# Performance work log

Hardware: AMD Instinct MI355X
Metric: run time of the kernel (lower is better)

The kernel has to match this reference:

```python
import jax, jax.numpy as jnp
import numpy as np

SEQLEN, BATCH, FEAT = 512, 64, 512
HID, WIN, LAYERS, OUT, NSPK = 1024, 16, 3, 512, 2


def setup_inputs() -> dict:
    key = jax.random.key(0)
    ks = jax.random.split(key, 16)
    s = 0.05  # small init scale to keep activations stable
    return {
        "h": jax.random.normal(ks[0], (SEQLEN, BATCH, FEAT), jnp.float32),
        "Wa": jax.random.normal(ks[1], (NSPK, HID, FEAT), jnp.float32) * s,
        "Wih0": jax.random.normal(ks[2], (4 * HID, FEAT), jnp.float32) * s,
        "Whh0": jax.random.normal(ks[3], (4 * HID, HID), jnp.float32) * s,
        "bih0": jax.random.normal(ks[4], (4 * HID,), jnp.float32) * s,
        "bhh0": jax.random.normal(ks[5], (4 * HID,), jnp.float32) * s,
        "Wih_rest": jax.random.normal(ks[6], (LAYERS - 1, 4 * HID, HID), jnp.float32) * s,
        "Whh_rest": jax.random.normal(ks[7], (LAYERS - 1, 4 * HID, HID), jnp.float32) * s,
        "bih_rest": jax.random.normal(ks[8], (LAYERS - 1, 4 * HID), jnp.float32) * s,
        "bhh_rest": jax.random.normal(ks[9], (LAYERS - 1, 4 * HID), jnp.float32) * s,
        "Wfc": jax.random.normal(ks[10], (OUT, HID + FEAT), jnp.float32) * s,
        "bfc": jax.random.normal(ks[11], (OUT,), jnp.float32) * s,
        "s0": jax.random.normal(ks[12], (BATCH, HID), jnp.float32),
        "h0": jax.random.normal(ks[13], (LAYERS, BATCH, HID), jnp.float32),
        "c0": jax.random.normal(ks[14], (LAYERS, BATCH, HID), jnp.float32),
    }


def _lstm_cell(x, h_prev, c_prev, Wih, Whh, bih, bhh):
    # torch.nn.LSTMCell math; only the new h is consumed downstream
    g = x @ Wih.T + bih + h_prev @ Whh.T + bhh  # [B, 4H]
    i, f, gg, o = jnp.split(g, 4, axis=1)
    c_new = jax.nn.sigmoid(f) * c_prev + jax.nn.sigmoid(i) * jnp.tanh(gg)
    return jax.nn.sigmoid(o) * jnp.tanh(c_new)


def reference(h, Wa, Wih0, Whh0, bih0, bhh0, Wih_rest, Whh_rest, bih_rest, bhh_rest, Wfc, bfc, s0, h0, c0):
    T, B, F = h.shape
    win_len = 2 * WIN + 1
    pad = jnp.zeros((WIN, B, F), h.dtype)
    h_pad = jnp.concatenate([pad, h, pad], axis=0)  # [T+2W, B, F]

    def make_step(Wa_s):
        def step(s_prev, i):
            window = jax.lax.dynamic_slice(h_pad, (i, 0, 0), (win_len, B, F))  # [w,B,F]
            proj = s_prev @ Wa_s                       # [B,F]
            e = jnp.einsum('bf,wbf->wb', proj, window)  # attention energies
            a = jax.nn.softmax(e, axis=0)
            c_t = jnp.einsum('wb,wbf->bf', a, window)   # context [B,F]
            x = _lstm_cell(c_t, h0[0], c0[0], Wih0, Whh0, bih0, bhh0)
            for l in range(Wih_rest.shape[0]):  # fixed small layer count
                x = _lstm_cell(x, h0[l + 1], c0[l + 1], Wih_rest[l], Whh_rest[l], bih_rest[l], bhh_rest[l])
            out = jax.nn.relu(jnp.concatenate([x, c_t], axis=1) @ Wfc.T + bfc)
            return x, out  # s_before for next step carries across speakers too
        return step

    outs = []
    s = s0
    for sp in range(Wa.shape[0]):
        s, o = jax.lax.scan(make_step(Wa[sp]), s, jnp.arange(T))
        outs.append(o)
    return jnp.stack(outs)  # [num_speaker, T, B, OUT]
```

## Files before the change

### kernel.cpp

```cpp
#include <hip/hip_runtime.h>

#define T_LEN 512
#define BATCH 64
#define FEATD 512
#define HID   1024
#define G4H   4096
#define WINR  16
#define WLEN  33
#define OUTD  512
#define CATD  1536
#define NBLK  256
#define NTHR  512

typedef unsigned int uint32;
typedef unsigned long long u64;
typedef unsigned short ushort16;
typedef short s16x8 __attribute__((ext_vector_type(8)));
typedef float f32x4 __attribute__((ext_vector_type(4)));

static const size_t OFF_U    = 0;
static const size_t OFF_HH   = 33554432;
static const size_t OFF_S    = OFF_HH + 786432;
static const size_t OFF_CB   = OFF_S  + 65536;
static const size_t OFF_X1   = OFF_CB + 16384;
static const size_t OFF_X2   = OFF_X1 + 32768;
static const size_t OFF_CK   = OFF_X2 + 32768;
static const size_t OFF_XK   = OFF_CK + 262144;
static const size_t OFF_BAR  = OFF_XK + 524288;
static const size_t OFF_WFCB = OFF_BAR + 1024;

__device__ __forceinline__ float sigmoidf_(float x) { return 1.0f / (1.0f + expf(-x)); }
__device__ __forceinline__ ushort16 f2bf(float f) {
  uint32 u = __float_as_uint(f);
  uint32 r = u + 0x7FFFu + ((u >> 16) & 1u);
  return (ushort16)(r >> 16);
}

__device__ __forceinline__ uint2 aload8(const void* p) {
  u64 v = __hip_atomic_load((const u64*)p, __ATOMIC_RELAXED, __HIP_MEMORY_SCOPE_AGENT);
  uint2 r; r.x = (unsigned)(v & 0xffffffffull); r.y = (unsigned)(v >> 32);
  return r;
}
__device__ __forceinline__ float aload4f(const void* p) {
  return __hip_atomic_load((const float*)p, __ATOMIC_RELAXED, __HIP_MEMORY_SCOPE_AGENT);
}
__device__ __forceinline__ void astore8(void* p, u64 v) {
  __hip_atomic_store((u64*)p, v, __ATOMIC_RELAXED, __HIP_MEMORY_SCOPE_AGENT);
}
__device__ __forceinline__ void astore4f(void* p, float v) {
  __hip_atomic_store((float*)p, v, __ATOMIC_RELAXED, __HIP_MEMORY_SCOPE_AGENT);
}

__device__ __forceinline__ void grid_barrier(unsigned* bar, unsigned epoch) {
  __syncthreads();
  if (threadIdx.x == 0) {
    unsigned* cnt  = bar + ((blockIdx.x & 7u) << 6);
    unsigned* gsum = bar + 512;
    unsigned a = __hip_atomic_fetch_add(cnt, 1u, __ATOMIC_RELAXED, __HIP_MEMORY_SCOPE_AGENT);
    if (((a + 1u) & 31u) == 0u)
      __hip_atomic_fetch_add(gsum, 1u, __ATOMIC_RELAXED, __HIP_MEMORY_SCOPE_AGENT);
    const unsigned target = epoch * 8u;
    while ((int)(__hip_atomic_load(gsum, __ATOMIC_RELAXED, __HIP_MEMORY_SCOPE_AGENT) - target) < 0)
      __builtin_amdgcn_s_sleep(2);
  }
  __syncthreads();
}

template<int KSTEPS>
__device__ __forceinline__ void lstm_stage_mfma(
    const ushort16* __restrict__ wl,
    const ushort16* __restrict__ actB4,
    const float* __restrict__ hhg,
    float c0v,
    ushort16* __restrict__ xoutB4,
    ushort16* __restrict__ xhist_slot,
    float* __restrict__ sOut,
    float* __restrict__ red,
    float* __restrict__ hv_l)
{
  const int tid  = threadIdx.x;
  const int wv   = tid >> 6;
  const int lane = tid & 63;
  const int nt   = wv & 3;
  const int kh   = wv >> 2;
  const int quad = lane >> 4;
  const int b    = nt * 16 + (lane & 15);
  const int half = KSTEPS / 2;

  f32x4 acc0 = {0.f, 0.f, 0.f, 0.f};
  f32x4 acc1 = {0.f, 0.f, 0.f, 0.f};
  #pragma unroll
  for (int i = 0; i < half; i += 2) {
    const int ks0 = kh * half + i;
    const int ks1 = ks0 + 1;
    s16x8 a0 = *(const s16x8*)(wl + ((size_t)ks0 * 64 + lane) * 8);
    s16x8 a1 = *(const s16x8*)(wl + ((size_t)ks1 * 64 + lane) * 8);
    const int g0 = ks0 * 8 + quad * 2;
    const int g1 = ks1 * 8 + quad * 2;
    uint2 lo0 = aload8(actB4 + ((size_t)g0 * 64 + b) * 4);
    uint2 hi0 = aload8(actB4 + ((size_t)(g0 + 1) * 64 + b) * 4);
    uint2 lo1 = aload8(actB4 + ((size_t)g1 * 64 + b) * 4);
    uint2 hi1 = aload8(actB4 + ((size_t)(g1 + 1) * 64 + b) * 4);
    union { uint4 u; s16x8 v; } b0, b1;
    b0.u = make_uint4(lo0.x, lo0.y, hi0.x, hi0.y);
    b1.u = make_uint4(lo1.x, lo1.y, hi1.x, hi1.y);
    acc0 = __builtin_amdgcn_mfma_f32_16x16x32_bf16(a0, b0.v, acc0, 0, 0, 0);
    acc1 = __builtin_amdgcn_mfma_f32_16x16x32_bf16(a1, b1.v, acc1, 0, 0, 0);
  }
  f32x4 acc = acc0 + acc1;
  {
    float* rp = red + (((size_t)(kh * 4 + nt) * 16 + quad * 4) * 16) + (lane & 15);
    rp[0]  = acc[0];
    rp[16] = acc[1];
    rp[32] = acc[2];
    rp[48] = acc[3];
  }
  __syncthreads();
  if (wv < 4) {
    const int jl = wv;
    const int bb = lane;
    const int ntb = bb >> 4, col = bb & 15;
    float g[4];
    #pragma unroll
    for (int gate = 0; gate < 4; ++gate) {
      const int m = gate * 4 + jl;
      g[gate] = red[((size_t)(0 + ntb) * 16 + m) * 16 + col]
              + red[((size_t)(4 + ntb) * 16 + m) * 16 + col]
              + hhg[gate];
    }
    float cn = sigmoidf_(g[1]) * c0v + sigmoidf_(g[0]) * tanhf(g[2]);
    float hv = sigmoidf_(g[3]) * tanhf(cn);
    if (sOut) astore4f(sOut + (size_t)bb * HID + (blockIdx.x << 2) + jl, hv);
    hv_l[jl * 64 + bb] = hv;
  }
  if (xoutB4 || xhist_slot) {
    __syncthreads();
    if (wv == 0) {
      const int bb = lane;
      uint32 lo = (uint32)f2bf(hv_l[0 * 64 + bb]) | ((uint32)f2bf(hv_l[1 * 64 + bb]) << 16);
      uint32 hi = (uint32)f2bf(hv_l[2 * 64 + bb]) | ((uint32)f2bf(hv_l[3 * 64 + bb]) << 16);
      u64 pk = ((u64)hi << 32) | (u64)lo;
      if (xoutB4)     astore8(xoutB4 + ((size_t)blockIdx.x * 64 + bb) * 4, pk);
      if (xhist_slot) astore8(xhist_slot + ((size_t)blockIdx.x * 64 + bb) * 4, pk);
    }
  }
}

__device__ __forceinline__ void fc_step_mfma(int tp, int sub,
    const ushort16* __restrict__ ch4,
    const ushort16* __restrict__ xh4,
    const ushort16* __restrict__ Wfcb,
    const float* __restrict__ bfc,
    float* __restrict__ outp, float* __restrict__ red)
{
  const int tid  = threadIdx.x;
  const int wv   = tid >> 6;
  const int lane = tid & 63;
  const int slot = tp & 15;
  const int ot   = sub >> 1;
  const int tsel = wv & 1;
  const int kq   = wv >> 1;
  const int quad = lane >> 4;
  const int b    = ((sub & 1) * 2 + tsel) * 16 + (lane & 15);
  const ushort16* xs = xh4 + (size_t)slot * 65536;
  const ushort16* cs = ch4 + (size_t)slot * 32768;
  const ushort16* wa = Wfcb + ((size_t)ot * 48 + (size_t)kq * 12) * 512;

  f32x4 acc0 = {0.f, 0.f, 0.f, 0.f};
  f32x4 acc1 = {0.f, 0.f, 0.f, 0.f};
  #pragma unroll
  for (int i = 0; i < 12; i += 2) {
    const int ks0 = kq * 12 + i;
    const int ks1 = ks0 + 1;
    s16x8 a0 = *(const s16x8*)(wa + (size_t)i * 512 + (size_t)lane * 8);
    s16x8 a1 = *(const s16x8*)(wa + (size_t)(i + 1) * 512 + (size_t)lane * 8);
    const ushort16* s0p = (ks0 < 32) ? xs : cs;
    const ushort16* s1p = (ks1 < 32) ? xs : cs;
    const int gg0 = ((ks0 < 32) ? ks0 * 8 : (ks0 - 32) * 8) + quad * 2;
    const int gg1 = ((ks1 < 32) ? ks1 * 8 : (ks1 - 32) * 8) + quad * 2;
    uint2 lo0 = aload8(s0p + ((size_t)gg0 * 64 + b) * 4);
    uint2 hi0 = aload8(s0p + ((size_t)(gg0 + 1) * 64 + b) * 4);
    uint2 lo1 = aload8(s1p + ((size_t)gg1 * 64 + b) * 4);
    uint2 hi1 = aload8(s1p + ((size_t)(gg1 + 1) * 64 + b) * 4);
    union { uint4 u; s16x8 v; } b0, b1;
    b0.u = make_uint4(lo0.x, lo0.y, hi0.x, hi0.y);
    b1.u = make_uint4(lo1.x, lo1.y, hi1.x, hi1.y);
    acc0 = __builtin_amdgcn_mfma_f32_16x16x32_bf16(a0, b0.v, acc0, 0, 0, 0);
    acc1 = __builtin_amdgcn_mfma_f32_16x16x32_bf16(a1, b1.v, acc1, 0, 0, 0);
  }
  f32x4 acc = acc0 + acc1;
  {
    float* rp = red + ((size_t)wv * 16 + quad * 4) * 16 + (lane & 15);
    rp[0]  = acc[0];
    rp[16] = acc[1];
    rp[32] = acc[2];
    rp[48] = acc[3];
  }
  __syncthreads();
  {
    const int tl   = tid >> 8;
    const int bcol = (tid >> 4) & 15;
    const int m    = tid & 15;
    float v = bfc[ot * 16 + m];
    #pragma unroll
    for (int k4 = 0; k4 < 4; ++k4)
      v += red[((size_t)(k4 * 2 + tl) * 16 + m) * 16 + bcol];
    const int bo = ((sub & 1) * 2 + tl) * 16 + bcol;
    outp[((size_t)tp * BATCH + bo) * OUTD + ot * 16 + m] = fmaxf(v, 0.f);
  }
}

__global__ void __launch_bounds__(NTHR)
decoder_kernel(const float* __restrict__ hin, const float* __restrict__ u,
               const float* __restrict__ Wih0, const float* __restrict__ Wihr,
               const ushort16* __restrict__ Wfcb, const float* __restrict__ bfc,
               const float* __restrict__ c0, const float* __restrict__ hhT,
               float* __restrict__ s,
               ushort16* __restrict__ x1B4, ushort16* __restrict__ x2B4,
               ushort16* __restrict__ chist4, ushort16* __restrict__ xhist4,
               unsigned* __restrict__ bar, float* __restrict__ outp)
{
  __shared__ ushort16 wlds[40960];
  __shared__ float s_l[HID];
  __shared__ float e_l[64];
  __shared__ float a_l[64];
  __shared__ float red[2 * 4 * 16 * 16];
  __shared__ float c_l[FEATD];
  __shared__ float hv_l[4 * 64];

  const int tid  = threadIdx.x;
  const int bid  = blockIdx.x;
  const int wv   = tid >> 6;
  const int lane = tid & 63;

  for (int r = tid; r < 40960; r += NTHR) {
    int local, ksz; const float* Wsrc;
    if (r < 8192)        { local = r;         ksz = FEATD; Wsrc = Wih0; }
    else if (r < 24576)  { local = r - 8192;  ksz = HID;   Wsrc = Wihr; }
    else                 { local = r - 24576; ksz = HID;   Wsrc = Wihr + (size_t)G4H * HID; }
    const int ks   = local >> 9;
    const int li   = local & 511;
    const int ln   = li >> 3;
    const int jj   = li & 7;
    const int m    = ln & 15;
    const int quad = ln >> 4;
    const int k    = ks * 32 + quad * 8 + jj;
    const int n    = (m >> 2) * HID + (bid << 2) + (m & 3);
    wlds[r] = f2bf(Wsrc[(size_t)n * ksz + k]);
  }

  float hh_r[3][4];
  float c0_r[3];
  if (wv < 4) {
    const int j  = (bid << 2) + wv;
    const int bb = lane;
    #pragma unroll
    for (int l = 0; l < 3; ++l) {
      #pragma unroll
      for (int gate = 0; gate < 4; ++gate)
        hh_r[l][gate] = hhT[((size_t)l * G4H + (size_t)gate * HID + j) * 64 + bb];
      c0_r[l] = c0[((size_t)l * BATCH + bb) * HID + j];
    }
  } else {
    #pragma unroll
    for (int l = 0; l < 3; ++l) {
      hh_r[l][0] = hh_r[l][1] = hh_r[l][2] = hh_r[l][3] = 0.f;
      c0_r[l] = 0.f;
    }
  }
  __syncthreads();

  unsigned ep = 0;
  for (int t = 0; t < T_LEN; ++t) {
    const int slot = t & 15;
    if (bid < BATCH) {
      const int b = bid;
      float pf0 = 0.f, pf1 = 0.f, pf2 = 0.f;
      {
        const int taun = t + 1 + WINR;
        if (taun < T_LEN) {
          pf0 = u[((size_t)taun * BATCH + b) * HID + tid];
          pf1 = u[((size_t)taun * BATCH + b) * HID + tid + NTHR];
          pf2 = hin[((size_t)taun * BATCH + b) * FEATD + tid];
        }
      }
      s_l[tid]        = aload4f(s + (size_t)b * HID + tid);
      s_l[tid + NTHR] = aload4f(s + (size_t)b * HID + tid + NTHR);
      __syncthreads();
      for (int w = wv; w < WLEN; w += 8) {
        const int tau = t + w - WINR;
        float e = 0.f;
        if (tau >= 0 && tau < T_LEN) {
          const float* up = u + ((size_t)tau * BATCH + b) * HID;
          #pragma unroll
          for (int i = 0; i < 16; ++i) {
            const int hidx = lane + (i << 6);
            e += s_l[hidx] * up[hidx];
          }
          #pragma unroll
          for (int m = 32; m; m >>= 1) e += __shfl_xor(e, m);
        }
        if (lane == 0) e_l[w] = e;
      }
      __syncthreads();
      if (tid < 64) {
        float e = (tid < WLEN) ? e_l[tid] : -1e30f;
        float mx = e;
        #pragma unroll
        for (int m = 32; m; m >>= 1) mx = fmaxf(mx, __shfl_xor(mx, m));
        float p = (tid < WLEN) ? expf(e - mx) : 0.f;
        float sm = p;
        #pragma unroll
        for (int m = 32; m; m >>= 1) sm += __shfl_xor(sm, m);
        if (tid < WLEN) a_l[tid] = p / sm;
      }
      __syncthreads();
      {
        const int w0 = (t < WINR) ? (WINR - t) : 0;
        const int w1 = (T_LEN + WINR - t < WLEN) ? (T_LEN + WINR - t) : WLEN;
        const size_t hstep = (size_t)BATCH * FEATD;
        const float* hp = hin + ((size_t)(t + w0 - WINR) * BATCH + b) * FEATD + tid;
        float c0a = 0.f, c1a = 0.f, c2a = 0.f, c3a = 0.f;
        int w = w0;
        for (; w + 3 < w1; w += 4) {
          c0a = fmaf(a_l[w],     hp[0],         c0a);
          c1a = fmaf(a_l[w + 1], hp[hstep],     c1a);
          c2a = fmaf(a_l[w + 2], hp[2 * hstep], c2a);
          c3a = fmaf(a_l[w + 3], hp[3 * hstep], c3a);
          hp += 4 * hstep;
        }
        for (; w < w1; ++w) { c0a = fmaf(a_l[w], hp[0], c0a); hp += hstep; }
        c_l[tid] = (c0a + c1a) + (c2a + c3a);
      }
      __syncthreads();
      if (tid < 128) {
        uint32 lo = (uint32)f2bf(c_l[4 * tid + 0]) | ((uint32)f2bf(c_l[4 * tid + 1]) << 16);
        uint32 hi = (uint32)f2bf(c_l[4 * tid + 2]) | ((uint32)f2bf(c_l[4 * tid + 3]) << 16);
        u64 pk = ((u64)hi << 32) | (u64)lo;
        astore8(chist4 + (size_t)slot * 32768 + ((size_t)tid * 64 + b) * 4, pk);
      }
      asm volatile("" :: "v"(pf0), "v"(pf1), "v"(pf2));
    } else if (t >= 3 && t % 3 == 0) {
      const int fb = bid - BATCH;
      const int tp = t - 3 + (fb >> 6);
      fc_step_mfma(tp, fb & 63, chist4, xhist4, Wfcb, bfc, outp, red);
    }
    grid_barrier(bar, ++ep);
    lstm_stage_mfma<16>(wlds, chist4 + (size_t)slot * 32768, hh_r[0], c0_r[0],
                        x1B4, nullptr, nullptr, red, hv_l);
    grid_barrier(bar, ++ep);
    lstm_stage_mfma<32>(wlds + 8192, x1B4, hh_r[1], c0_r[1],
                        x2B4, nullptr, nullptr, red, hv_l);
    grid_barrier(bar, ++ep);
    lstm_stage_mfma<32>(wlds + 24576, x2B4, hh_r[2], c0_r[2],
                        nullptr, xhist4 + (size_t)slot * 65536, s, red, hv_l);
    grid_barrier(bar, ++ep);
  }
  if (bid < 128) {
    const int tp = 510 + (bid >> 6);
    fc_step_mfma(tp, bid & 63, chist4, xhist4, Wfcb, bfc, outp, red);
  }
}

__global__ void __launch_bounds__(256)
barreset_kernel(unsigned* __restrict__ bar)
{
  for (int i = threadIdx.x; i < 1024; i += 256) bar[i] = 0u;
}

__global__ void __launch_bounds__(256)
wfcswz_kernel(const float* __restrict__ Wfc, ushort16* __restrict__ Wfcb)
{
  const int idx = blockIdx.x * 256 + threadIdx.x;
  const int ot  = idx / 24576;
  const int r   = idx - ot * 24576;
  const int ks  = r >> 9;
  const int li  = r & 511;
  const int ln  = li >> 3;
  const int j   = li & 7;
  const int k   = ks * 32 + (ln >> 4) * 8 + j;
  const int o   = ot * 16 + (ln & 15);
  Wfcb[idx] = f2bf(Wfc[(size_t)o * CATD + k]);
}

__global__ void __launch_bounds__(256)
gemm_u_kernel(const float* __restrict__ A, const float* __restrict__ Bm,
              float* __restrict__ C)
{
  __shared__ float Al[64 * 68];
  __shared__ float Bl[64 * 68];
  const int tid = threadIdx.x;
  const int m0 = blockIdx.x * 64;
  const int n0 = blockIdx.y * 64;
  const int tx = tid & 15, ty = tid >> 4;
  float acc[4][4] = {};
  for (int kc = 0; kc < 512; kc += 64) {
    #pragma unroll
    for (int p = 0; p < 4; ++p) {
      const int row = p * 16 + (tid >> 4);
      const int kq  = (tid & 15) * 4;
      float4 v = *(const float4*)(A + (size_t)(m0 + row) * 512 + kc + kq);
      Al[(kq + 0) * 68 + row] = v.x;
      Al[(kq + 1) * 68 + row] = v.y;
      Al[(kq + 2) * 68 + row] = v.z;
      Al[(kq + 3) * 68 + row] = v.w;
      float4 w = *(const float4*)(Bm + (size_t)(n0 + row) * 512 + kc + kq);
      Bl[(kq + 0) * 68 + row] = w.x;
      Bl[(kq + 1) * 68 + row] = w.y;
      Bl[(kq + 2) * 68 + row] = w.z;
      Bl[(kq + 3) * 68 + row] = w.w;
    }
    __syncthreads();
    #pragma unroll 8
    for (int k = 0; k < 64; ++k) {
      float4 av = *(const float4*)(&Al[k * 68 + ty * 4]);
      float4 bv = *(const float4*)(&Bl[k * 68 + tx * 4]);
      float aa[4] = {av.x, av.y, av.z, av.w};
      float bb[4] = {bv.x, bv.y, bv.z, bv.w};
      #pragma unroll
      for (int i = 0; i < 4; ++i)
        #pragma unroll
        for (int jj = 0; jj < 4; ++jj)
          acc[i][jj] = fmaf(aa[i], bb[jj], acc[i][jj]);
    }
    __syncthreads();
  }
  #pragma unroll
  for (int i = 0; i < 4; ++i) {
    float4 r = {acc[i][0], acc[i][1], acc[i][2], acc[i][3]};
    *(float4*)(C + (size_t)(m0 + ty * 4 + i) * 1024 + n0 + tx * 4) = r;
  }
}

__global__ void __launch_bounds__(256)
hhconst_kernel(const float* __restrict__ Whh0, const float* __restrict__ Whr,
               const float* __restrict__ bih0, const float* __restrict__ bhh0,
               const float* __restrict__ bihr, const float* __restrict__ bhhr,
               const float* __restrict__ h0, float* __restrict__ hh)
{
  const int idx = blockIdx.x * 256 + threadIdx.x;
  const int b = idx & 63;
  const int n = (idx >> 6) & 4095;
  const int l = idx >> 18;
  const float* W = (l == 0) ? (Whh0 + (size_t)n * HID)
                            : (Whr + ((size_t)(l - 1) * G4H + n) * HID);
  float acc = ((l == 0) ? bih0[n] : bihr[(l - 1) * G4H + n])
            + ((l == 0) ? bhh0[n] : bhhr[(l - 1) * G4H + n]);
  const float* hr = h0 + ((size_t)l * BATCH + b) * HID;
  #pragma unroll 2
  for (int k = 0; k < HID; k += 4) {
    float4 a4 = *(const float4*)(hr + k);
    float4 w4 = *(const float4*)(W + k);
    acc += a4.x * w4.x + a4.y * w4.y + a4.z * w4.z + a4.w * w4.w;
  }
  hh[idx] = acc;
}

__global__ void __launch_bounds__(256)
init_kernel(const float* __restrict__ s0, float* __restrict__ s, unsigned* __restrict__ bar)
{
  const int gid = blockIdx.x * 256 + threadIdx.x;
  if (gid < BATCH * HID) s[gid] = s0[gid];
  if (blockIdx.x == 0)
    for (int i = threadIdx.x; i < 1024; i += 256) bar[i] = 0u;
}

extern "C" void kernel_launch(void* const* d_in, const int* in_sizes, int n_in,
                              void* d_out, int out_size, void* d_ws, size_t ws_size,
                              hipStream_t stream) {
  (void)in_sizes; (void)n_in; (void)out_size; (void)ws_size;
  const float* h    = (const float*)d_in[0];
  const float* Wa   = (const float*)d_in[1];
  const float* Wih0 = (const float*)d_in[2];
  const float* Whh0 = (const float*)d_in[3];
  const float* bih0 = (const float*)d_in[4];
  const float* bhh0 = (const float*)d_in[5];
  const float* Wihr = (const float*)d_in[6];
  const float* Whhr = (const float*)d_in[7];
  const float* bihr = (const float*)d_in[8];
  const float* bhhr = (const float*)d_in[9];
  const float* Wfc  = (const float*)d_in[10];
  const float* bfc  = (const float*)d_in[11];
  const float* s0   = (const float*)d_in[12];
  const float* h0   = (const float*)d_in[13];
  const float* c0   = (const float*)d_in[14];
  float* out = (float*)d_out;
  float* ws  = (float*)d_ws;

  float* u         = ws + OFF_U;
  float* hhT       = ws + OFF_HH;
  float* s         = ws + OFF_S;
  ushort16* x1B4   = (ushort16*)(ws + OFF_X1);
  ushort16* x2B4   = (ushort16*)(ws + OFF_X2);
  ushort16* chist4 = (ushort16*)(ws + OFF_CK);
  ushort16* xhist4 = (ushort16*)(ws + OFF_XK);
  unsigned* bar    = (unsigned*)(ws + OFF_BAR);
  ushort16* Wfcb   = (ushort16*)(ws + OFF_WFCB);

  hipLaunchKernelGGL(init_kernel, dim3(256), dim3(256), 0, stream, s0, s, bar);
  hipLaunchKernelGGL(hhconst_kernel, dim3(3072), dim3(256), 0, stream,
                     Whh0, Whhr, bih0, bhh0, bihr, bhhr, h0, hhT);
  hipLaunchKernelGGL(wfcswz_kernel, dim3(3072), dim3(256), 0, stream, Wfc, Wfcb);
  for (int sp = 0; sp < 2; ++sp) {
    hipLaunchKernelGGL(gemm_u_kernel, dim3(512, 16), dim3(256), 0, stream,
                       h, Wa + (size_t)sp * HID * FEATD, u);
    hipLaunchKernelGGL(barreset_kernel, dim3(1), dim3(256), 0, stream, bar);
    hipLaunchKernelGGL(decoder_kernel, dim3(NBLK), dim3(NTHR), 0, stream,
                       h, u, Wih0, Wihr, Wfcb, bfc, c0, hhT, s,
                       x1B4, x2B4, chist4, xhist4, bar,
                       out + (size_t)sp * T_LEN * BATCH * OUTD);
  }
}
```

Baseline: 36.42 ms.

## Add sharded release flags to grid barrier and pack LSTM outputs via shuffles

The grid barrier now has the last arriving group leader write the epoch into 16 separate release flags. Each block spins on its own flag instead of all 256 blocks polling one global counter, which reduces contention on that cache line. The LSTM gate epilogue is also remapped so four adjacent lanes hold the four hidden units of a batch row. The bf16 outputs are packed with warp shuffles, removing an LDS round-trip and one __syncthreads per stage. Barrier storage grows, and the reset kernels clear the larger region.

```diff
diff --git a/kernel.cpp b/kernel.cpp
--- a/kernel.cpp
+++ b/kernel.cpp
@@ -27,7 +27,7 @@
 static const size_t OFF_CK   = OFF_X2 + 32768;
 static const size_t OFF_XK   = OFF_CK + 262144;
 static const size_t OFF_BAR  = OFF_XK + 524288;
-static const size_t OFF_WFCB = OFF_BAR + 1024;
+static const size_t OFF_WFCB = OFF_BAR + 2048;
 
 __device__ __forceinline__ float sigmoidf_(float x) { return 1.0f / (1.0f + expf(-x)); }
 __device__ __forceinline__ ushort16 f2bf(float f) {
@@ -56,12 +56,19 @@
   if (threadIdx.x == 0) {
     unsigned* cnt  = bar + ((blockIdx.x & 7u) << 6);
     unsigned* gsum = bar + 512;
+    unsigned* rel  = bar + 576;
     unsigned a = __hip_atomic_fetch_add(cnt, 1u, __ATOMIC_RELAXED, __HIP_MEMORY_SCOPE_AGENT);
-    if (((a + 1u) & 31u) == 0u)
-      __hip_atomic_fetch_add(gsum, 1u, __ATOMIC_RELAXED, __HIP_MEMORY_SCOPE_AGENT);
-    const unsigned target = epoch * 8u;
-    while ((int)(__hip_atomic_load(gsum, __ATOMIC_RELAXED, __HIP_MEMORY_SCOPE_AGENT) - target) < 0)
-      __builtin_amdgcn_s_sleep(2);
+    if (((a + 1u) & 31u) == 0u) {
+      unsigned og = __hip_atomic_fetch_add(gsum, 1u, __ATOMIC_RELAXED, __HIP_MEMORY_SCOPE_AGENT);
+      if (og + 1u == epoch * 8u) {
+        #pragma unroll
+        for (int i = 0; i < 16; ++i)
+          __hip_atomic_store(rel + i * 32, epoch, __ATOMIC_RELAXED, __HIP_MEMORY_SCOPE_AGENT);
+      }
+    }
+    unsigned* myrel = rel + (blockIdx.x & 15u) * 32;
+    while ((int)(__hip_atomic_load(myrel, __ATOMIC_RELAXED, __HIP_MEMORY_SCOPE_AGENT) - epoch) < 0)
+      __builtin_amdgcn_s_sleep(1);
   }
   __syncthreads();
 }
@@ -75,8 +82,7 @@
     ushort16* __restrict__ xoutB4,
     ushort16* __restrict__ xhist_slot,
     float* __restrict__ sOut,
-    float* __restrict__ red,
-    float* __restrict__ hv_l)
+    float* __restrict__ red)
 {
   const int tid  = threadIdx.x;
   const int wv   = tid >> 6;
@@ -117,9 +123,10 @@
   }
   __syncthreads();
   if (wv < 4) {
-    const int jl = wv;
-    const int bb = lane;
-    const int ntb = bb >> 4, col = bb & 15;
+    const int jl  = lane & 3;
+    const int bb  = wv * 16 + (lane >> 2);
+    const int ntb = bb >> 4;
+    const int col = bb & 15;
     float g[4];
     #pragma unroll
     for (int gate = 0; gate < 4; ++gate) {
@@ -131,17 +138,15 @@
     float cn = sigmoidf_(g[1]) * c0v + sigmoidf_(g[0]) * tanhf(g[2]);
     float hv = sigmoidf_(g[3]) * tanhf(cn);
     if (sOut) astore4f(sOut + (size_t)bb * HID + (blockIdx.x << 2) + jl, hv);
-    hv_l[jl * 64 + bb] = hv;
-  }
-  if (xoutB4 || xhist_slot) {
-    __syncthreads();
-    if (wv == 0) {
-      const int bb = lane;
-      uint32 lo = (uint32)f2bf(hv_l[0 * 64 + bb]) | ((uint32)f2bf(hv_l[1 * 64 + bb]) << 16);
-      uint32 hi = (uint32)f2bf(hv_l[2 * 64 + bb]) | ((uint32)f2bf(hv_l[3 * 64 + bb]) << 16);
-      u64 pk = ((u64)hi << 32) | (u64)lo;
-      if (xoutB4)     astore8(xoutB4 + ((size_t)blockIdx.x * 64 + bb) * 4, pk);
-      if (xhist_slot) astore8(xhist_slot + ((size_t)blockIdx.x * 64 + bb) * 4, pk);
+    if (xoutB4 || xhist_slot) {
+      uint32 my = ((uint32)f2bf(hv)) << ((jl & 1) * 16);
+      uint32 pair = my | (uint32)__shfl_xor((int)my, 1);
+      uint32 other = (uint32)__shfl_xor((int)pair, 2);
+      if (jl == 0) {
+        u64 pk = ((u64)other << 32) | (u64)pair;
+        if (xoutB4)     astore8(xoutB4 + ((size_t)blockIdx.x * 64 + bb) * 4, pk);
+        if (xhist_slot) astore8(xhist_slot + ((size_t)blockIdx.x * 64 + bb) * 4, pk);
+      }
     }
   }
 }
@@ -226,7 +231,6 @@
   __shared__ float a_l[64];
   __shared__ float red[2 * 4 * 16 * 16];
   __shared__ float c_l[FEATD];
-  __shared__ float hv_l[4 * 64];
 
   const int tid  = threadIdx.x;
   const int bid  = blockIdx.x;
@@ -252,8 +256,9 @@
   float hh_r[3][4];
   float c0_r[3];
   if (wv < 4) {
-    const int j  = (bid << 2) + wv;
-    const int bb = lane;
+    const int jl = lane & 3;
+    const int bb = wv * 16 + (lane >> 2);
+    const int j  = (bid << 2) + jl;
     #pragma unroll
     for (int l = 0; l < 3; ++l) {
       #pragma unroll
@@ -347,13 +352,13 @@
     }
     grid_barrier(bar, ++ep);
     lstm_stage_mfma<16>(wlds, chist4 + (size_t)slot * 32768, hh_r[0], c0_r[0],
-                        x1B4, nullptr, nullptr, red, hv_l);
+                        x1B4, nullptr, nullptr, red);
     grid_barrier(bar, ++ep);
     lstm_stage_mfma<32>(wlds + 8192, x1B4, hh_r[1], c0_r[1],
-                        x2B4, nullptr, nullptr, red, hv_l);
+                        x2B4, nullptr, nullptr, red);
     grid_barrier(bar, ++ep);
     lstm_stage_mfma<32>(wlds + 24576, x2B4, hh_r[2], c0_r[2],
-                        nullptr, xhist4 + (size_t)slot * 65536, s, red, hv_l);
+                        nullptr, xhist4 + (size_t)slot * 65536, s, red);
     grid_barrier(bar, ++ep);
   }
   if (bid < 128) {
@@ -365,7 +370,7 @@
 __global__ void __launch_bounds__(256)
 barreset_kernel(unsigned* __restrict__ bar)
 {
-  for (int i = threadIdx.x; i < 1024; i += 256) bar[i] = 0u;
+  for (int i = threadIdx.x; i < 2048; i += 256) bar[i] = 0u;
 }
 
 __global__ void __launch_bounds__(256)
@@ -462,7 +467,7 @@
   const int gid = blockIdx.x * 256 + threadIdx.x;
   if (gid < BATCH * HID) s[gid] = s0[gid];
   if (blockIdx.x == 0)
-    for (int i = threadIdx.x; i < 1024; i += 256) bar[i] = 0u;
+    for (int i = threadIdx.x; i < 2048; i += 256) bar[i] = 0u;
 }
 
 extern "C" void kernel_launch(void* const* d_in, const int* in_sizes, int n_in,
```

After: 35.00 ms. 3.9% less time.
